# Performance work log

Hardware: AMD Instinct MI355X
Metric: run time of the kernel (lower is better)

The kernel has to match this reference:

```python
import jax, jax.numpy as jnp
import numpy as np

V, D, A = 100000, 128, 64
L, N, K = 3, 20000, 16


def setup_inputs() -> dict:
    key = jax.random.key(0)
    k1, k2, k3, k4, k5, k6 = jax.random.split(key, 6)
    Leaf_emb = jax.random.normal(k1, (V, D), dtype=jnp.float32)
    nodes = jax.random.randint(k2, (L, N), 0, V, dtype=jnp.int32)
    neighbors = jax.random.randint(k3, (L, N, K), 0, V, dtype=jnp.int32)
    masks = jnp.zeros((L, N, K), dtype=jnp.float32)  # additive mask, 0 = valid
    weights = jax.random.normal(k4, (L, N, K), dtype=jnp.float32)
    W_att = jax.random.uniform(k5, (2 * D, A), dtype=jnp.float32)
    b_att = jnp.zeros((A,), dtype=jnp.float32)
    v_att = jax.random.uniform(k6, (A,), dtype=jnp.float32)
    return {"Leaf_emb": Leaf_emb, "nodes": nodes, "neighbors": neighbors,
            "masks": masks, "weights": weights,
            "W_att": W_att, "b_att": b_att, "v_att": v_att}


def reference(Leaf_emb, nodes, neighbors, masks, weights, W_att, b_att, v_att):
    # Sequential over L tree levels (fixed, small): each level gathers node and
    # neighbor embeddings, scores neighbors with a 2-layer attention MLP,
    # combines masked-softmax attention with softmax'd structural weights,
    # sums neighbor embeddings and scatters the result back into W_tmp.
    W_tmp = Leaf_emb
    n_levels = nodes.shape[0]
    for i in range(n_levels):
        node = nodes[i]                      # [N] (constant across K in original)
        neighbor = neighbors[i]              # [N, K]
        mask = masks[i]                      # [N, K] additive
        weight = weights[i]                  # [N, K]
        node_tmp = Leaf_emb[node][:, None, :]          # [N, 1, D] from ORIGINAL emb
        neighbor_tmp = W_tmp[neighbor]                 # [N, K, D] from running emb
        node_b = jnp.broadcast_to(node_tmp, neighbor_tmp.shape)
        att_in = jnp.concatenate([node_b, neighbor_tmp], axis=2)  # [N, K, 2D]
        mlp = jax.nn.leaky_relu(att_in @ W_att + b_att, 0.01)     # [N, K, A]
        pre = mlp @ v_att                                         # [N, K]
        att = jax.nn.softmax(pre + mask, axis=1) * jax.nn.softmax(weight, axis=1)
        temp_emb = jnp.einsum('nkd,nk->nd', neighbor_tmp, att)    # [N, D]
        W_tmp = W_tmp.at[node].set(temp_emb)
    return W_tmp
```

## Files before the change

### kernel.cpp

```cpp
#include <hip/hip_runtime.h>
#include <math.h>

#define V 100000
#define D 128
#define A 64
#define LVLS 3
#define NN 20000
#define KK 16
#define BK 32
#define ASTRIDE 34
#define BSTRIDE 68
#define PSTRIDE 128

__global__ __launch_bounds__(256, 2)
void projall_kernel(const float* __restrict__ Leaf, const float* __restrict__ Watt,
                    const float* __restrict__ batt, float* __restrict__ projAll,
                    float* __restrict__ outp) {
    __shared__ float As[128 * ASTRIDE];
    __shared__ float Bs[BK * BSTRIDE];
    int t = threadIdx.x;
    int tx = t & 15, ty = t >> 4;
    int r0 = blockIdx.x * 128;
    int half = blockIdx.y;
    const float* Wmat = Watt + (size_t)half * D * A;

    const float* srcp[4];
    int rg[4];
#pragma unroll
    for (int jj = 0; jj < 4; ++jj) {
        int r = r0 + (t >> 3) + 32 * jj;
        rg[jj] = r;
        int rr = r < V ? r : V - 1;
        srcp[jj] = Leaf + (size_t)rr * D + ((t & 7) << 2);
    }

    float4 bv = make_float4(0.f, 0.f, 0.f, 0.f);
    if (half == 0) bv = *(const float4*)(batt + 4 * tx);
    float acc[8][4];
#pragma unroll
    for (int i = 0; i < 8; ++i) {
        acc[i][0] = bv.x; acc[i][1] = bv.y; acc[i][2] = bv.z; acc[i][3] = bv.w;
    }

    for (int k0 = 0; k0 < D; k0 += BK) {
#pragma unroll
        for (int jj = 0; jj < 4; ++jj) {
            float4 v = *(const float4*)(srcp[jj] + k0);
            *(float4*)&As[((t >> 3) + 32 * jj) * ASTRIDE + ((t & 7) << 2)] = v;
            if (half == 0 && rg[jj] < V)
                *(float4*)(outp + (size_t)rg[jj] * D + k0 + ((t & 7) << 2)) = v;
        }
#pragma unroll
        for (int ss = 0; ss < 2; ++ss) {
            int s = t + 256 * ss;
            int kB = s >> 4, c4 = (s & 15) << 2;
            *(float4*)&Bs[kB * BSTRIDE + c4] =
                *(const float4*)(Wmat + (size_t)(k0 + kB) * A + c4);
        }
        __syncthreads();
#pragma unroll
        for (int kc = 0; kc < BK; kc += 4) {
            float4 b0 = *(const float4*)&Bs[(kc + 0) * BSTRIDE + 4 * tx];
            float4 b1 = *(const float4*)&Bs[(kc + 1) * BSTRIDE + 4 * tx];
            float4 b2 = *(const float4*)&Bs[(kc + 2) * BSTRIDE + 4 * tx];
            float4 b3 = *(const float4*)&Bs[(kc + 3) * BSTRIDE + 4 * tx];
#pragma unroll
            for (int i = 0; i < 8; ++i) {
                float4 a = *(const float4*)&As[(8 * ty + i) * ASTRIDE + kc];
                acc[i][0] = fmaf(a.x, b0.x, acc[i][0]);
                acc[i][0] = fmaf(a.y, b1.x, acc[i][0]);
                acc[i][0] = fmaf(a.z, b2.x, acc[i][0]);
                acc[i][0] = fmaf(a.w, b3.x, acc[i][0]);
                acc[i][1] = fmaf(a.x, b0.y, acc[i][1]);
                acc[i][1] = fmaf(a.y, b1.y, acc[i][1]);
                acc[i][1] = fmaf(a.z, b2.y, acc[i][1]);
                acc[i][1] = fmaf(a.w, b3.y, acc[i][1]);
                acc[i][2] = fmaf(a.x, b0.z, acc[i][2]);
                acc[i][2] = fmaf(a.y, b1.z, acc[i][2]);
                acc[i][2] = fmaf(a.z, b2.z, acc[i][2]);
                acc[i][2] = fmaf(a.w, b3.z, acc[i][2]);
                acc[i][3] = fmaf(a.x, b0.w, acc[i][3]);
                acc[i][3] = fmaf(a.y, b1.w, acc[i][3]);
                acc[i][3] = fmaf(a.z, b2.w, acc[i][3]);
                acc[i][3] = fmaf(a.w, b3.w, acc[i][3]);
            }
        }
        __syncthreads();
    }

#pragma unroll
    for (int i = 0; i < 8; ++i) {
        int gr = r0 + 8 * ty + i;
        if (gr < V) {
            float4 o = make_float4(acc[i][0], acc[i][1], acc[i][2], acc[i][3]);
            *(float4*)(projAll + (size_t)gr * PSTRIDE + half * 64 + 4 * tx) = o;
        }
    }
}

__global__ __launch_bounds__(256, 2)
void commit_kernel(const float* __restrict__ tmp, const float* __restrict__ Wmat,
                   const int* __restrict__ nodes_l, const int* __restrict__ claim,
                   float* __restrict__ outp, float* __restrict__ projAll, int do_proj) {
    __shared__ float As[128 * ASTRIDE];
    __shared__ float Bs[BK * BSTRIDE];
    int t = threadIdx.x;
    int tx = t & 15, ty = t >> 4;
    int r0 = blockIdx.x * 128;

    const float* srcp[4];
    int vrow[4], win[4];
#pragma unroll
    for (int jj = 0; jj < 4; ++jj) {
        int r = r0 + (t >> 3) + 32 * jj;
        int rr = r < NN ? r : NN - 1;
        srcp[jj] = tmp + (size_t)rr * D + ((t & 7) << 2);
        int v = nodes_l[rr];
        vrow[jj] = v;
        win[jj] = (r < NN) && (claim[v] == rr);
    }

    float acc[8][4];
#pragma unroll
    for (int i = 0; i < 8; ++i) {
        acc[i][0] = 0.f; acc[i][1] = 0.f; acc[i][2] = 0.f; acc[i][3] = 0.f;
    }

    for (int k0 = 0; k0 < D; k0 += BK) {
#pragma unroll
        for (int jj = 0; jj < 4; ++jj) {
            float4 v = *(const float4*)(srcp[jj] + k0);
            *(float4*)&As[((t >> 3) + 32 * jj) * ASTRIDE + ((t & 7) << 2)] = v;
            if (win[jj])
                *(float4*)(outp + (size_t)vrow[jj] * D + k0 + ((t & 7) << 2)) = v;
        }
        if (do_proj) {
#pragma unroll
            for (int ss = 0; ss < 2; ++ss) {
                int s = t + 256 * ss;
                int kB = s >> 4, c4 = (s & 15) << 2;
                *(float4*)&Bs[kB * BSTRIDE + c4] =
                    *(const float4*)(Wmat + (size_t)(k0 + kB) * A + c4);
            }
        }
        __syncthreads();
        if (do_proj) {
#pragma unroll
            for (int kc = 0; kc < BK; kc += 4) {
                float4 b0 = *(const float4*)&Bs[(kc + 0) * BSTRIDE + 4 * tx];
                float4 b1 = *(const float4*)&Bs[(kc + 1) * BSTRIDE + 4 * tx];
                float4 b2 = *(const float4*)&Bs[(kc + 2) * BSTRIDE + 4 * tx];
                float4 b3 = *(const float4*)&Bs[(kc + 3) * BSTRIDE + 4 * tx];
#pragma unroll
                for (int i = 0; i < 8; ++i) {
                    float4 a = *(const float4*)&As[(8 * ty + i) * ASTRIDE + kc];
                    acc[i][0] = fmaf(a.x, b0.x, acc[i][0]);
                    acc[i][0] = fmaf(a.y, b1.x, acc[i][0]);
                    acc[i][0] = fmaf(a.z, b2.x, acc[i][0]);
                    acc[i][0] = fmaf(a.w, b3.x, acc[i][0]);
                    acc[i][1] = fmaf(a.x, b0.y, acc[i][1]);
                    acc[i][1] = fmaf(a.y, b1.y, acc[i][1]);
                    acc[i][1] = fmaf(a.z, b2.y, acc[i][1]);
                    acc[i][1] = fmaf(a.w, b3.y, acc[i][1]);
                    acc[i][2] = fmaf(a.x, b0.z, acc[i][2]);
                    acc[i][2] = fmaf(a.y, b1.z, acc[i][2]);
                    acc[i][2] = fmaf(a.z, b2.z, acc[i][2]);
                    acc[i][2] = fmaf(a.w, b3.z, acc[i][2]);
                    acc[i][3] = fmaf(a.x, b0.w, acc[i][3]);
                    acc[i][3] = fmaf(a.y, b1.w, acc[i][3]);
                    acc[i][3] = fmaf(a.z, b2.w, acc[i][3]);
                    acc[i][3] = fmaf(a.w, b3.w, acc[i][3]);
                }
            }
        }
        __syncthreads();
    }

    if (do_proj) {
#pragma unroll
        for (int i = 0; i < 8; ++i) {
            int gr = r0 + 8 * ty + i;
            if (gr < NN) {
                int v = nodes_l[gr];
                if (claim[v] == gr) {
                    float4 o = make_float4(acc[i][0], acc[i][1], acc[i][2], acc[i][3]);
                    *(float4*)(projAll + (size_t)v * PSTRIDE + 64 + 4 * tx) = o;
                }
            }
        }
    }
}

__global__ __launch_bounds__(256)
void attn_kernel(const float* __restrict__ Wc, const float* __restrict__ projAll,
                 const int* __restrict__ nodes_l, const int* __restrict__ neigh,
                 const float* __restrict__ maskp, const float* __restrict__ weightp,
                 const float* __restrict__ v_att, float* __restrict__ tmp) {
    int lane = threadIdx.x & 63;
    int n = blockIdx.x * 4 + (threadIdx.x >> 6);
    int k16 = lane & 15, q = lane >> 4;

    int   vnode = nodes_l[n];
    int   nbk = neigh[n * KK + k16];
    float wv  = weightp[n * KK + k16];
    float mk  = maskp[n * KK + k16];

    const float* npr = projAll + (size_t)vnode * PSTRIDE + q * 16;
    const float* var = v_att + q * 16;
    const float* pr  = projAll + (size_t)nbk * PSTRIDE + 64 + q * 16;

    float part = 0.f;
#pragma unroll
    for (int j = 0; j < 16; j += 4) {
        float4 npv = *(const float4*)(npr + j);
        float4 vav = *(const float4*)(var + j);
        float4 pv  = *(const float4*)(pr + j);
        float x;
        x = npv.x + pv.x; x = fmaxf(x, 0.01f * x); part = fmaf(x, vav.x, part);
        x = npv.y + pv.y; x = fmaxf(x, 0.01f * x); part = fmaf(x, vav.y, part);
        x = npv.z + pv.z; x = fmaxf(x, 0.01f * x); part = fmaf(x, vav.z, part);
        x = npv.w + pv.w; x = fmaxf(x, 0.01f * x); part = fmaf(x, vav.w, part);
    }
    part += __shfl_xor(part, 16);
    part += __shfl_xor(part, 32);
    float pre = part + mk;

    float mp = pre, mw = wv;
#pragma unroll
    for (int off = 8; off >= 1; off >>= 1) {
        mp = fmaxf(mp, __shfl_xor(mp, off));
        mw = fmaxf(mw, __shfl_xor(mw, off));
    }
    float ep = __expf(pre - mp), ew = __expf(wv - mw);
    float sp = ep, sw = ew;
#pragma unroll
    for (int off = 8; off >= 1; off >>= 1) {
        sp += __shfl_xor(sp, off);
        sw += __shfl_xor(sw, off);
    }
    float att = (ep / sp) * (ew / sw);

    int half = lane >> 5, li = lane & 31;
    float ax = 0.f, ay = 0.f, az = 0.f, aw = 0.f;
#pragma unroll
    for (int m = 0; m < 8; ++m) {
        int src = 2 * m + half;
        int nb   = __shfl(nbk, src);
        float ak = __shfl(att, src);
        float4 e = *(const float4*)&Wc[(size_t)nb * D + 4 * li];
        ax = fmaf(e.x, ak, ax); ay = fmaf(e.y, ak, ay);
        az = fmaf(e.z, ak, az); aw = fmaf(e.w, ak, aw);
    }
    ax += __shfl_xor(ax, 32); ay += __shfl_xor(ay, 32);
    az += __shfl_xor(az, 32); aw += __shfl_xor(aw, 32);
    if (half == 0) {
        float4 o = make_float4(ax, ay, az, aw);
        *(float4*)&tmp[(size_t)n * D + 4 * li] = o;
    }
}

__global__ void amax3_kernel(const int* __restrict__ nodes, int* __restrict__ claims, int total) {
    int i = blockIdx.x * 256 + threadIdx.x;
    if (i < total) {
        int lvl = i / NN, pos = i - lvl * NN;
        atomicMax(&claims[(size_t)lvl * V + nodes[i]], pos);
    }
}

extern "C" void kernel_launch(void* const* d_in, const int* in_sizes, int n_in,
                              void* d_out, int out_size, void* d_ws, size_t ws_size,
                              hipStream_t stream) {
    const float* Leaf    = (const float*)d_in[0];
    const int*   nodes   = (const int*)d_in[1];
    const int*   neigh   = (const int*)d_in[2];
    const float* masks   = (const float*)d_in[3];
    const float* weights = (const float*)d_in[4];
    const float* Watt    = (const float*)d_in[5];
    const float* batt    = (const float*)d_in[6];
    const float* vatt    = (const float*)d_in[7];
    float* out = (float*)d_out;

    char* ws = (char*)d_ws;
    float* projAll = (float*)ws;
    float* tmp     = (float*)(ws + (size_t)V * PSTRIDE * 4);
    int*   claims  = (int*)(ws + (size_t)(V * PSTRIDE + NN * D) * 4);

    hipMemsetAsync(claims, 0xFF, (size_t)LVLS * V * sizeof(int), stream);
    amax3_kernel<<<(LVLS * NN + 255) / 256, 256, 0, stream>>>(nodes, claims, LVLS * NN);
    projall_kernel<<<dim3((V + 127) / 128, 2), 256, 0, stream>>>(
        Leaf, Watt, batt, projAll, out);

    for (int l = 0; l < LVLS; ++l) {
        const int* nodes_l = nodes + l * NN;
        attn_kernel<<<NN / 4, 256, 0, stream>>>(out, projAll, nodes_l,
                                                neigh + (size_t)l * NN * KK,
                                                masks + (size_t)l * NN * KK,
                                                weights + (size_t)l * NN * KK, vatt, tmp);
        commit_kernel<<<(NN + 127) / 128, 256, 0, stream>>>(
            tmp, Watt + (size_t)D * A, nodes_l, claims + (size_t)l * V, out, projAll,
            (l + 1 < LVLS) ? 1 : 0);
    }
}
```

Before: 324.6 us.

## Register-prefetch next K tile and shrink tiles in projection and commit GEMMs

Both small GEMM kernels now load the next K slice into registers while computing the current one, with K tile cut from 32 to 16 and one barrier removed per iteration. The commit kernel halves its row tile to 64 rows, launching more blocks for the 20000-row problem, and launch bounds ask for 4 blocks per CU. This is meant to hide global load latency and raise occupancy, at the cost of more loop iterations and barriers per unit of work.

```diff
diff --git a/kernel.cpp b/kernel.cpp
--- a/kernel.cpp
+++ b/kernel.cpp
@@ -7,32 +7,36 @@
 #define LVLS 3
 #define NN 20000
 #define KK 16
-#define BK 32
-#define ASTRIDE 34
-#define BSTRIDE 68
+#define BK2 16
+#define AST2 18
+#define BST2 68
 #define PSTRIDE 128
 
-__global__ __launch_bounds__(256, 2)
+__global__ __launch_bounds__(256, 4)
 void projall_kernel(const float* __restrict__ Leaf, const float* __restrict__ Watt,
                     const float* __restrict__ batt, float* __restrict__ projAll,
                     float* __restrict__ outp) {
-    __shared__ float As[128 * ASTRIDE];
-    __shared__ float Bs[BK * BSTRIDE];
+    __shared__ float As[128 * AST2];
+    __shared__ float Bs[BK2 * BST2];
     int t = threadIdx.x;
     int tx = t & 15, ty = t >> 4;
     int r0 = blockIdx.x * 128;
     int half = blockIdx.y;
     const float* Wmat = Watt + (size_t)half * D * A;
 
-    const float* srcp[4];
-    int rg[4];
-#pragma unroll
-    for (int jj = 0; jj < 4; ++jj) {
-        int r = r0 + (t >> 3) + 32 * jj;
-        rg[jj] = r;
+    int ar = t >> 2;
+    int ak = (t & 3) << 2;
+    const float* asrc[2];
+    int arow[2];
+#pragma unroll
+    for (int jj = 0; jj < 2; ++jj) {
+        int r = r0 + ar + 64 * jj;
+        arow[jj] = r;
         int rr = r < V ? r : V - 1;
-        srcp[jj] = Leaf + (size_t)rr * D + ((t & 7) << 2);
-    }
+        asrc[jj] = Leaf + (size_t)rr * D + ak;
+    }
+    int bk = t >> 4;
+    int bc = (t & 15) << 2;
 
     float4 bv = make_float4(0.f, 0.f, 0.f, 0.f);
     if (half == 0) bv = *(const float4*)(batt + 4 * tx);
@@ -42,31 +46,35 @@
         acc[i][0] = bv.x; acc[i][1] = bv.y; acc[i][2] = bv.z; acc[i][3] = bv.w;
     }
 
-    for (int k0 = 0; k0 < D; k0 += BK) {
-#pragma unroll
-        for (int jj = 0; jj < 4; ++jj) {
-            float4 v = *(const float4*)(srcp[jj] + k0);
-            *(float4*)&As[((t >> 3) + 32 * jj) * ASTRIDE + ((t & 7) << 2)] = v;
-            if (half == 0 && rg[jj] < V)
-                *(float4*)(outp + (size_t)rg[jj] * D + k0 + ((t & 7) << 2)) = v;
-        }
-#pragma unroll
-        for (int ss = 0; ss < 2; ++ss) {
-            int s = t + 256 * ss;
-            int kB = s >> 4, c4 = (s & 15) << 2;
-            *(float4*)&Bs[kB * BSTRIDE + c4] =
-                *(const float4*)(Wmat + (size_t)(k0 + kB) * A + c4);
+    float4 pa0 = *(const float4*)(asrc[0]);
+    float4 pa1 = *(const float4*)(asrc[1]);
+    float4 pb  = *(const float4*)(Wmat + (size_t)bk * A + bc);
+
+    for (int k0 = 0; k0 < D; k0 += BK2) {
+        if (k0) __syncthreads();
+        *(float4*)&As[(ar +  0) * AST2 + ak] = pa0;
+        *(float4*)&As[(ar + 64) * AST2 + ak] = pa1;
+        *(float4*)&Bs[bk * BST2 + bc] = pb;
+        if (half == 0) {
+            if (arow[0] < V) *(float4*)(outp + (size_t)arow[0] * D + k0 + ak) = pa0;
+            if (arow[1] < V) *(float4*)(outp + (size_t)arow[1] * D + k0 + ak) = pa1;
         }
         __syncthreads();
-#pragma unroll
-        for (int kc = 0; kc < BK; kc += 4) {
-            float4 b0 = *(const float4*)&Bs[(kc + 0) * BSTRIDE + 4 * tx];
-            float4 b1 = *(const float4*)&Bs[(kc + 1) * BSTRIDE + 4 * tx];
-            float4 b2 = *(const float4*)&Bs[(kc + 2) * BSTRIDE + 4 * tx];
-            float4 b3 = *(const float4*)&Bs[(kc + 3) * BSTRIDE + 4 * tx];
+        int kn = k0 + BK2;
+        if (kn < D) {
+            pa0 = *(const float4*)(asrc[0] + kn);
+            pa1 = *(const float4*)(asrc[1] + kn);
+            pb  = *(const float4*)(Wmat + (size_t)(kn + bk) * A + bc);
+        }
+#pragma unroll
+        for (int kc = 0; kc < BK2; kc += 4) {
+            float4 b0 = *(const float4*)&Bs[(kc + 0) * BST2 + 4 * tx];
+            float4 b1 = *(const float4*)&Bs[(kc + 1) * BST2 + 4 * tx];
+            float4 b2 = *(const float4*)&Bs[(kc + 2) * BST2 + 4 * tx];
+            float4 b3 = *(const float4*)&Bs[(kc + 3) * BST2 + 4 * tx];
 #pragma unroll
             for (int i = 0; i < 8; ++i) {
-                float4 a = *(const float4*)&As[(8 * ty + i) * ASTRIDE + kc];
+                float4 a = *(const float4*)&As[(8 * ty + i) * AST2 + kc];
                 acc[i][0] = fmaf(a.x, b0.x, acc[i][0]);
                 acc[i][0] = fmaf(a.y, b1.x, acc[i][0]);
                 acc[i][0] = fmaf(a.z, b2.x, acc[i][0]);
@@ -85,7 +93,6 @@
                 acc[i][3] = fmaf(a.w, b3.w, acc[i][3]);
             }
         }
-        __syncthreads();
     }
 
 #pragma unroll
@@ -98,62 +105,59 @@
     }
 }
 
-__global__ __launch_bounds__(256, 2)
+__global__ __launch_bounds__(256, 4)
 void commit_kernel(const float* __restrict__ tmp, const float* __restrict__ Wmat,
                    const int* __restrict__ nodes_l, const int* __restrict__ claim,
                    float* __restrict__ outp, float* __restrict__ projAll, int do_proj) {
-    __shared__ float As[128 * ASTRIDE];
-    __shared__ float Bs[BK * BSTRIDE];
+    __shared__ float As[64 * AST2];
+    __shared__ float Bs[BK2 * BST2];
     int t = threadIdx.x;
     int tx = t & 15, ty = t >> 4;
-    int r0 = blockIdx.x * 128;
-
-    const float* srcp[4];
-    int vrow[4], win[4];
-#pragma unroll
-    for (int jj = 0; jj < 4; ++jj) {
-        int r = r0 + (t >> 3) + 32 * jj;
-        int rr = r < NN ? r : NN - 1;
-        srcp[jj] = tmp + (size_t)rr * D + ((t & 7) << 2);
-        int v = nodes_l[rr];
-        vrow[jj] = v;
-        win[jj] = (r < NN) && (claim[v] == rr);
-    }
-
-    float acc[8][4];
-#pragma unroll
-    for (int i = 0; i < 8; ++i) {
+    int r0 = blockIdx.x * 64;
+
+    int ar = t >> 2;
+    int ak = (t & 3) << 2;
+    int r = r0 + ar;
+    int rr = r < NN ? r : NN - 1;
+    const float* asrc = tmp + (size_t)rr * D + ak;
+    int vrow = nodes_l[rr];
+    int win = (r < NN) && (claim[vrow] == rr);
+
+    int bk = t >> 4;
+    int bc = (t & 15) << 2;
+
+    float acc[4][4];
+#pragma unroll
+    for (int i = 0; i < 4; ++i) {
         acc[i][0] = 0.f; acc[i][1] = 0.f; acc[i][2] = 0.f; acc[i][3] = 0.f;
     }
 
-    for (int k0 = 0; k0 < D; k0 += BK) {
-#pragma unroll
-        for (int jj = 0; jj < 4; ++jj) {
-            float4 v = *(const float4*)(srcp[jj] + k0);
-            *(float4*)&As[((t >> 3) + 32 * jj) * ASTRIDE + ((t & 7) << 2)] = v;
-            if (win[jj])
-                *(float4*)(outp + (size_t)vrow[jj] * D + k0 + ((t & 7) << 2)) = v;
+    float4 pa = *(const float4*)(asrc);
+    float4 pb = make_float4(0.f, 0.f, 0.f, 0.f);
+    if (do_proj) pb = *(const float4*)(Wmat + (size_t)bk * A + bc);
+
+    for (int k0 = 0; k0 < D; k0 += BK2) {
+        if (k0) __syncthreads();
+        *(float4*)&As[ar * AST2 + ak] = pa;
+        if (do_proj) *(float4*)&Bs[bk * BST2 + bc] = pb;
+        if (win)
+            *(float4*)(outp + (size_t)vrow * D + k0 + ak) = pa;
+        __syncthreads();
+        int kn = k0 + BK2;
+        if (kn < D) {
+            pa = *(const float4*)(asrc + kn);
+            if (do_proj) pb = *(const float4*)(Wmat + (size_t)(kn + bk) * A + bc);
         }
         if (do_proj) {
 #pragma unroll
-            for (int ss = 0; ss < 2; ++ss) {
-                int s = t + 256 * ss;
-                int kB = s >> 4, c4 = (s & 15) << 2;
-                *(float4*)&Bs[kB * BSTRIDE + c4] =
-                    *(const float4*)(Wmat + (size_t)(k0 + kB) * A + c4);
-            }
-        }
-        __syncthreads();
-        if (do_proj) {
-#pragma unroll
-            for (int kc = 0; kc < BK; kc += 4) {
-                float4 b0 = *(const float4*)&Bs[(kc + 0) * BSTRIDE + 4 * tx];
-                float4 b1 = *(const float4*)&Bs[(kc + 1) * BSTRIDE + 4 * tx];
-                float4 b2 = *(const float4*)&Bs[(kc + 2) * BSTRIDE + 4 * tx];
-                float4 b3 = *(const float4*)&Bs[(kc + 3) * BSTRIDE + 4 * tx];
-#pragma unroll
-                for (int i = 0; i < 8; ++i) {
-                    float4 a = *(const float4*)&As[(8 * ty + i) * ASTRIDE + kc];
+            for (int kc = 0; kc < BK2; kc += 4) {
+                float4 b0 = *(const float4*)&Bs[(kc + 0) * BST2 + 4 * tx];
+                float4 b1 = *(const float4*)&Bs[(kc + 1) * BST2 + 4 * tx];
+                float4 b2 = *(const float4*)&Bs[(kc + 2) * BST2 + 4 * tx];
+                float4 b3 = *(const float4*)&Bs[(kc + 3) * BST2 + 4 * tx];
+#pragma unroll
+                for (int i = 0; i < 4; ++i) {
+                    float4 a = *(const float4*)&As[(4 * ty + i) * AST2 + kc];
                     acc[i][0] = fmaf(a.x, b0.x, acc[i][0]);
                     acc[i][0] = fmaf(a.y, b1.x, acc[i][0]);
                     acc[i][0] = fmaf(a.z, b2.x, acc[i][0]);
@@ -173,13 +177,12 @@
                 }
             }
         }
-        __syncthreads();
     }
 
     if (do_proj) {
 #pragma unroll
-        for (int i = 0; i < 8; ++i) {
-            int gr = r0 + 8 * ty + i;
+        for (int i = 0; i < 4; ++i) {
+            int gr = r0 + 4 * ty + i;
             if (gr < NN) {
                 int v = nodes_l[gr];
                 if (claim[v] == gr) {
@@ -296,7 +299,7 @@
                                                 neigh + (size_t)l * NN * KK,
                                                 masks + (size_t)l * NN * KK,
                                                 weights + (size_t)l * NN * KK, vatt, tmp);
-        commit_kernel<<<(NN + 127) / 128, 256, 0, stream>>>(
+        commit_kernel<<<(NN + 63) / 64, 256, 0, stream>>>(
             tmp, Watt + (size_t)D * A, nodes_l, claims + (size_t)l * V, out, projAll,
             (l + 1 < LVLS) ? 1 : 0);
     }
```

Measured after the change: 305.3 us. 5.9% less time.
